# Kernel optimization log

Hardware: AMD Instinct MI355X
Metric: run time of the kernel (lower is better)

## Reference

```python
import jax, jax.numpy as jnp
import numpy as np

D_PROJ = 256
SCALE = D_PROJ ** (-0.5)


def setup_inputs() -> dict:
    key = jax.random.key(0)
    k1, k2, k3, k4 = jax.random.split(key, 4)
    B, L, Dh = 16, 2048, 1280
    T, Dg = 512, 768
    H = jax.random.normal(k1, (B, L, Dh), dtype=jnp.float32)
    G = jax.random.normal(k2, (B, T, Dg), dtype=jnp.float32)
    # Linear weights (torch nn.Linear: out = x @ W.T), small init to keep softmax well-conditioned
    Wq = jax.random.normal(k3, (D_PROJ, Dg), dtype=jnp.float32) * 0.02
    Wk = jax.random.normal(k4, (D_PROJ, Dh), dtype=jnp.float32) * 0.02
    return {"H": H, "G": G, "Wq": Wq, "Wk": Wk}


def reference(H, G, Wq, Wk):
    # Q = Wq(G): [B,T,P]; K = Wk(H): [B,L,P]
    Q = jnp.einsum('btg,pg->btp', G, Wq)
    K = jnp.einsum('bld,pd->blp', H, Wk)
    # The torch module's chunked online-softmax computes exact softmax over L.
    logits = jnp.einsum('btp,blp->btl', Q, K) * SCALE  # [B,T,L]
    A = jax.nn.softmax(logits, axis=-1)
    # Values are the raw residue embeddings H (not projected).
    Z = jnp.einsum('btl,bld->btd', A, H)  # [B,T,Dh]
    return Z
```

## Files before the change

### kernel.cpp

```cpp
#include <hip/hip_runtime.h>
#include <stdint.h>

typedef __attribute__((ext_vector_type(8))) short   short8;
typedef __attribute__((ext_vector_type(8))) __bf16  bf16x8;
typedef __attribute__((ext_vector_type(4))) float   floatx4;

#define DEV static __device__ __forceinline__

DEV unsigned short f2b(float f) {
  union { float f; unsigned u; } v; v.f = f;
  unsigned u = v.u;
  unsigned r = u + 0x7FFFu + ((u >> 16) & 1u);
  return (unsigned short)(r >> 16);
}
DEV float b2f(unsigned short s) {
  union { unsigned u; float f; } v; v.u = ((unsigned)s) << 16;
  return v.f;
}

DEV void gload_lds16(const void* g, void* l) {
  __builtin_amdgcn_global_load_lds(
      (const __attribute__((address_space(1))) unsigned int*)g,
      (__attribute__((address_space(3))) unsigned int*)l,
      16, 0, 0);
}

__global__ void cvt_kernel(const float* __restrict__ in, unsigned short* __restrict__ out, int n4) {
  int i = blockIdx.x * blockDim.x + threadIdx.x;
  if (i >= n4) return;
  float4 v = ((const float4*)in)[i];
  ushort4 o;
  o.x = f2b(v.x); o.y = f2b(v.y); o.z = f2b(v.z); o.w = f2b(v.w);
  ((ushort4*)out)[i] = o;
}

__global__ void transpose_cvt_H(const float* __restrict__ H, unsigned short* __restrict__ HT) {
  __shared__ unsigned short tile[64 * 68];
  const int b  = blockIdx.z;
  const int l0 = blockIdx.x * 64;
  const int d0 = blockIdx.y * 64;
  const int t  = threadIdx.x;

  {
    int row = t >> 2;
    int seg = t & 3;
    const float* src = H + ((size_t)b * 2048 + l0 + row) * 1280 + d0 + seg * 16;
#pragma unroll
    for (int s = 0; s < 4; ++s) {
      float4 v = *(const float4*)(src + s * 4);
      ushort4 o;
      o.x = f2b(v.x); o.y = f2b(v.y); o.z = f2b(v.z); o.w = f2b(v.w);
      *(ushort4*)&tile[row * 68 + seg * 16 + s * 4] = o;
    }
  }
  __syncthreads();
  {
    int dr = t >> 2;
    int ls = (t & 3) * 16;
    unsigned short* dst = HT + ((size_t)b * 1280 + d0 + dr) * 2048 + l0 + ls;
    short8 a, c;
#pragma unroll
    for (int i = 0; i < 8; ++i) a[i] = (short)tile[(ls + i) * 68 + dr];
#pragma unroll
    for (int i = 0; i < 8; ++i) c[i] = (short)tile[(ls + 8 + i) * 68 + dr];
    *(short8*)dst = a;
    *(short8*)(dst + 8) = c;
  }
}

__global__ void rowsum_inv_kernel(const unsigned short* __restrict__ E, float* __restrict__ linv, int rowlen) {
  int row  = blockIdx.x * 4 + (threadIdx.x >> 6);
  int lane = threadIdx.x & 63;
  const unsigned short* p = E + (size_t)row * rowlen;
  float s = 0.f;
  for (int c = lane * 8; c < rowlen; c += 512) {
    short8 v = *(const short8*)(p + c);
#pragma unroll
    for (int k = 0; k < 8; ++k) s += b2f((unsigned short)v[k]);
  }
#pragma unroll
  for (int off = 32; off > 0; off >>= 1) s += __shfl_down(s, off, 64);
  if (lane == 0) linv[row] = 1.0f / s;
}

template <int AMODE>
__global__ void proj_gemm(const void* __restrict__ Apv, const unsigned short* __restrict__ Bt,
                          unsigned short* __restrict__ C, int K, int lda) {
  __shared__ unsigned short As[64 * 32];
  __shared__ unsigned short Bs[256 * 32];

  const int m0   = blockIdx.x * 64;
  const int t    = threadIdx.x;
  const int lane = t & 63;
  const int wave = t >> 6;
  const int wn   = wave * 64;
  const int r16  = lane & 15;
  const int q    = lane >> 4;

  const unsigned short* Abf = (const unsigned short*)Apv;
  const float* A32 = (const float*)Apv;

  floatx4 acc[4][4];
#pragma unroll
  for (int i = 0; i < 4; ++i)
#pragma unroll
    for (int j = 0; j < 4; ++j) acc[i][j] = (floatx4){0.f, 0.f, 0.f, 0.f};

  for (int kt = 0; kt < K; kt += 32) {
    __syncthreads();
#pragma unroll
    for (int cc = 0; cc < 4; ++cc) {
      int c = t + cc * 256;
      gload_lds16(Bt + (size_t)(c >> 2) * K + kt + (c & 3) * 8, &Bs[c * 8]);
    }
    if constexpr (AMODE == 0) {
      gload_lds16(Abf + (size_t)(m0 + (t >> 2)) * lda + kt + (t & 3) * 8, &As[t * 8]);
    } else {
      const float* g = A32 + (size_t)(m0 + (t >> 2)) * lda + kt + (t & 3) * 8;
      float4 v0 = *(const float4*)g;
      float4 v1 = *(const float4*)(g + 4);
      short8 p;
      p[0] = (short)f2b(v0.x); p[1] = (short)f2b(v0.y);
      p[2] = (short)f2b(v0.z); p[3] = (short)f2b(v0.w);
      p[4] = (short)f2b(v1.x); p[5] = (short)f2b(v1.y);
      p[6] = (short)f2b(v1.z); p[7] = (short)f2b(v1.w);
      *(short8*)&As[t * 8] = p;
    }
    __syncthreads();

    bf16x8 af[4], bfr[4];
#pragma unroll
    for (int i = 0; i < 4; ++i) af[i]  = *(const bf16x8*)&As[(i * 16 + r16) * 32 + q * 8];
#pragma unroll
    for (int j = 0; j < 4; ++j) bfr[j] = *(const bf16x8*)&Bs[(wn + j * 16 + r16) * 32 + q * 8];
#pragma unroll
    for (int i = 0; i < 4; ++i)
#pragma unroll
      for (int j = 0; j < 4; ++j)
        acc[i][j] = __builtin_amdgcn_mfma_f32_16x16x32_bf16(af[i], bfr[j], acc[i][j], 0, 0, 0);
  }

#pragma unroll
  for (int i = 0; i < 4; ++i) {
#pragma unroll
    for (int r = 0; r < 4; ++r) {
      int m = m0 + i * 16 + q * 4 + r;
#pragma unroll
      for (int j = 0; j < 4; ++j) {
        int n = wn + j * 16 + r16;
        C[(size_t)m * 256 + n] = f2b(acc[i][j][r]);
      }
    }
  }
}

template <int EPI>
__global__ void gemm_nt(const unsigned short* __restrict__ Ab, const unsigned short* __restrict__ Btb,
                        void* __restrict__ Cpv, const float* __restrict__ linvb,
                        int K, int lda, int ldb, int ldc,
                        long long sA, long long sB, long long sC, int sL, float escale) {
  __shared__ unsigned short As[128 * 32];
  __shared__ unsigned short Bs[128 * 32];

  const int bz  = blockIdx.z;
  const int m0  = blockIdx.y * 128;
  const int n0  = blockIdx.x * 128;
  const int t   = threadIdx.x;
  const int lane = t & 63;
  const int wave = t >> 6;
  const int wm  = (wave & 1) * 64;
  const int wn  = (wave >> 1) * 64;
  const int r16 = lane & 15;
  const int q   = lane >> 4;

  const unsigned short* Bt = Btb + (long long)bz * sB;
  const unsigned short* A  = Ab + (long long)bz * sA;

  floatx4 acc[4][4];
#pragma unroll
  for (int i = 0; i < 4; ++i)
#pragma unroll
    for (int j = 0; j < 4; ++j) acc[i][j] = (floatx4){0.f, 0.f, 0.f, 0.f};

  for (int kt = 0; kt < K; kt += 32) {
    __syncthreads();
#pragma unroll
    for (int cc = 0; cc < 2; ++cc) {
      int c = t + cc * 256;
      gload_lds16(Bt + (size_t)(n0 + (c >> 2)) * ldb + kt + (c & 3) * 8, &Bs[c * 8]);
    }
#pragma unroll
    for (int cc = 0; cc < 2; ++cc) {
      int c = t + cc * 256;
      gload_lds16(A + (size_t)(m0 + (c >> 2)) * lda + kt + (c & 3) * 8, &As[c * 8]);
    }
    __syncthreads();

    bf16x8 af[4], bfr[4];
#pragma unroll
    for (int i = 0; i < 4; ++i) af[i]  = *(const bf16x8*)&As[(wm + i * 16 + r16) * 32 + q * 8];
#pragma unroll
    for (int j = 0; j < 4; ++j) bfr[j] = *(const bf16x8*)&Bs[(wn + j * 16 + r16) * 32 + q * 8];
#pragma unroll
    for (int i = 0; i < 4; ++i)
#pragma unroll
      for (int j = 0; j < 4; ++j)
        acc[i][j] = __builtin_amdgcn_mfma_f32_16x16x32_bf16(af[i], bfr[j], acc[i][j], 0, 0, 0);
  }

  if constexpr (EPI == 1) {
    unsigned short* C = (unsigned short*)Cpv + (long long)bz * sC;
#pragma unroll
    for (int i = 0; i < 4; ++i) {
#pragma unroll
      for (int r = 0; r < 4; ++r) {
        int m = m0 + wm + i * 16 + q * 4 + r;
#pragma unroll
        for (int j = 0; j < 4; ++j) {
          int n = n0 + wn + j * 16 + r16;
          C[(size_t)m * ldc + n] = f2b(__expf(acc[i][j][r] * escale));
        }
      }
    }
  } else {
    float* C = (float*)Cpv + (long long)bz * sC;
    const float* linv = linvb + (long long)bz * sL;
#pragma unroll
    for (int i = 0; i < 4; ++i) {
#pragma unroll
      for (int r = 0; r < 4; ++r) {
        int m = m0 + wm + i * 16 + q * 4 + r;
        float sc = linv[m];
#pragma unroll
        for (int j = 0; j < 4; ++j) {
          int n = n0 + wn + j * 16 + r16;
          C[(size_t)m * ldc + n] = acc[i][j][r] * sc;
        }
      }
    }
  }
}

extern "C" void kernel_launch(void* const* d_in, const int* in_sizes, int n_in,
                              void* d_out, int out_size, void* d_ws, size_t ws_size,
                              hipStream_t stream) {
  (void)in_sizes; (void)n_in; (void)out_size; (void)ws_size;
  const float* H  = (const float*)d_in[0];
  const float* G  = (const float*)d_in[1];
  const float* Wq = (const float*)d_in[2];
  const float* Wk = (const float*)d_in[3];
  float* Z = (float*)d_out;

  constexpr int B = 16, L = 2048, Dh = 1280, T = 512, Dg = 768, P = 256;

  char* ws = (char*)d_ws;
  size_t off = 0;
  auto alloc = [&](size_t bytes) { void* p = ws + off; off += (bytes + 255) & ~(size_t)255; return p; };
  unsigned short* Gbf  = (unsigned short*)alloc((size_t)B * T * Dg * 2);
  unsigned short* Wqbf = (unsigned short*)alloc((size_t)P * Dg * 2);
  unsigned short* Wkbf = (unsigned short*)alloc((size_t)P * Dh * 2);
  unsigned short* Qbf  = (unsigned short*)alloc((size_t)B * T * P * 2);
  unsigned short* Kbf  = (unsigned short*)alloc((size_t)B * L * P * 2);
  unsigned short* HT   = (unsigned short*)alloc((size_t)B * Dh * L * 2);
  unsigned short* E    = (unsigned short*)alloc((size_t)B * T * L * 2);
  float*          linv = (float*)alloc((size_t)B * T * 4);

  cvt_kernel<<<(B * T * Dg / 4 + 255) / 256, 256, 0, stream>>>(G, Gbf, B * T * Dg / 4);
  cvt_kernel<<<(P * Dg / 4 + 255) / 256, 256, 0, stream>>>(Wq, Wqbf, P * Dg / 4);
  cvt_kernel<<<(P * Dh / 4 + 255) / 256, 256, 0, stream>>>(Wk, Wkbf, P * Dh / 4);
  transpose_cvt_H<<<dim3(L / 64, Dh / 64, B), 256, 0, stream>>>(H, HT);

  proj_gemm<0><<<B * T / 64, 256, 0, stream>>>(Gbf, Wqbf, Qbf, Dg, Dg);
  proj_gemm<1><<<B * L / 64, 256, 0, stream>>>(H, Wkbf, Kbf, Dh, Dh);
  gemm_nt<1><<<dim3(L / 128, T / 128, B), 256, 0, stream>>>(
      Qbf, Kbf, E, nullptr, P, P, P, L,
      (long long)T * P, (long long)L * P, (long long)T * L, 0, 0.0625f);
  rowsum_inv_kernel<<<B * T / 4, 256, 0, stream>>>(E, linv, L);
  gemm_nt<2><<<dim3(Dh / 128, T / 128, B), 256, 0, stream>>>(
      E, HT, Z, linv, P * 0 + L, L, L, Dh,
      (long long)T * L, (long long)Dh * L, (long long)T * Dh, T, 0.f);
}
```

Baseline: 472.8 us.

## Fuse softmax row sums into exp GEMM epilogue and remap blocks per XCD

After: 444.2 us. 6.1% less time.

```diff
diff --git a/kernel.cpp b/kernel.cpp
--- a/kernel.cpp
+++ b/kernel.cpp
@@ -13,10 +13,6 @@
   unsigned r = u + 0x7FFFu + ((u >> 16) & 1u);
   return (unsigned short)(r >> 16);
 }
-DEV float b2f(unsigned short s) {
-  union { unsigned u; float f; } v; v.u = ((unsigned)s) << 16;
-  return v.f;
-}
 
 DEV void gload_lds16(const void* g, void* l) {
   __builtin_amdgcn_global_load_lds(
@@ -25,17 +21,28 @@
       16, 0, 0);
 }
 
-__global__ void cvt_kernel(const float* __restrict__ in, unsigned short* __restrict__ out, int n4) {
+__global__ void cvt3_kernel(const float* __restrict__ a, unsigned short* __restrict__ oa, int na4,
+                            const float* __restrict__ b, unsigned short* __restrict__ ob, int nb4,
+                            const float* __restrict__ c, unsigned short* __restrict__ oc, int nc4) {
   int i = blockIdx.x * blockDim.x + threadIdx.x;
-  if (i >= n4) return;
-  float4 v = ((const float4*)in)[i];
+  const float* src; unsigned short* dst; int k;
+  if (i < na4)                { src = a; dst = oa; k = i; }
+  else if (i < na4 + nb4)     { src = b; dst = ob; k = i - na4; }
+  else if (i < na4 + nb4 + nc4) { src = c; dst = oc; k = i - na4 - nb4; }
+  else return;
+  float4 v = ((const float4*)src)[k];
   ushort4 o;
   o.x = f2b(v.x); o.y = f2b(v.y); o.z = f2b(v.z); o.w = f2b(v.w);
-  ((ushort4*)out)[i] = o;
+  ((ushort4*)dst)[k] = o;
+}
+
+__global__ void zero_kernel(float* __restrict__ p, int n) {
+  int i = blockIdx.x * blockDim.x + threadIdx.x;
+  if (i < n) p[i] = 0.f;
 }
 
 __global__ void transpose_cvt_H(const float* __restrict__ H, unsigned short* __restrict__ HT) {
-  __shared__ unsigned short tile[64 * 68];
+  __shared__ unsigned short tile[64 * 66];
   const int b  = blockIdx.z;
   const int l0 = blockIdx.x * 64;
   const int d0 = blockIdx.y * 64;
@@ -45,12 +52,14 @@
     int row = t >> 2;
     int seg = t & 3;
     const float* src = H + ((size_t)b * 2048 + l0 + row) * 1280 + d0 + seg * 16;
+    unsigned short* trow = &tile[row * 66 + seg * 16];
 #pragma unroll
     for (int s = 0; s < 4; ++s) {
       float4 v = *(const float4*)(src + s * 4);
-      ushort4 o;
-      o.x = f2b(v.x); o.y = f2b(v.y); o.z = f2b(v.z); o.w = f2b(v.w);
-      *(ushort4*)&tile[row * 68 + seg * 16 + s * 4] = o;
+      ushort2 p0 = { f2b(v.x), f2b(v.y) };
+      ushort2 p1 = { f2b(v.z), f2b(v.w) };
+      *(ushort2*)&trow[s * 4]     = p0;
+      *(ushort2*)&trow[s * 4 + 2] = p1;
     }
   }
   __syncthreads();
@@ -60,27 +69,12 @@
     unsigned short* dst = HT + ((size_t)b * 1280 + d0 + dr) * 2048 + l0 + ls;
     short8 a, c;
 #pragma unroll
-    for (int i = 0; i < 8; ++i) a[i] = (short)tile[(ls + i) * 68 + dr];
-#pragma unroll
-    for (int i = 0; i < 8; ++i) c[i] = (short)tile[(ls + 8 + i) * 68 + dr];
+    for (int i = 0; i < 8; ++i) a[i] = (short)tile[(ls + i) * 66 + dr];
+#pragma unroll
+    for (int i = 0; i < 8; ++i) c[i] = (short)tile[(ls + 8 + i) * 66 + dr];
     *(short8*)dst = a;
     *(short8*)(dst + 8) = c;
   }
-}
-
-__global__ void rowsum_inv_kernel(const unsigned short* __restrict__ E, float* __restrict__ linv, int rowlen) {
-  int row  = blockIdx.x * 4 + (threadIdx.x >> 6);
-  int lane = threadIdx.x & 63;
-  const unsigned short* p = E + (size_t)row * rowlen;
-  float s = 0.f;
-  for (int c = lane * 8; c < rowlen; c += 512) {
-    short8 v = *(const short8*)(p + c);
-#pragma unroll
-    for (int k = 0; k < 8; ++k) s += b2f((unsigned short)v[k]);
-  }
-#pragma unroll
-  for (int off = 32; off > 0; off >>= 1) s += __shfl_down(s, off, 64);
-  if (lane == 0) linv[row] = 1.0f / s;
 }
 
 template <int AMODE>
@@ -156,22 +150,28 @@
 
 template <int EPI>
 __global__ void gemm_nt(const unsigned short* __restrict__ Ab, const unsigned short* __restrict__ Btb,
-                        void* __restrict__ Cpv, const float* __restrict__ linvb,
+                        void* __restrict__ Cpv, float* __restrict__ sums,
                         int K, int lda, int ldb, int ldc,
-                        long long sA, long long sB, long long sC, int sL, float escale) {
+                        long long sA, long long sB, long long sC, int sstride,
+                        float escale, int nx, int tiles_pb) {
   __shared__ unsigned short As[128 * 32];
   __shared__ unsigned short Bs[128 * 32];
 
-  const int bz  = blockIdx.z;
-  const int m0  = blockIdx.y * 128;
-  const int n0  = blockIdx.x * 128;
-  const int t   = threadIdx.x;
+  const int g   = blockIdx.x;
+  const int xcd = g & 7;
+  const int jj  = g >> 3;
+  const int bz  = xcd * 2 + jj / tiles_pb;
+  const int tt  = jj % tiles_pb;
+  const int m0  = (tt / nx) * 128;
+  const int n0  = (tt % nx) * 128;
+
+  const int t    = threadIdx.x;
   const int lane = t & 63;
   const int wave = t >> 6;
-  const int wm  = (wave & 1) * 64;
-  const int wn  = (wave >> 1) * 64;
-  const int r16 = lane & 15;
-  const int q   = lane >> 4;
+  const int wm   = (wave & 1) * 64;
+  const int wn   = (wave >> 1) * 64;
+  const int r16  = lane & 15;
+  const int q    = lane >> 4;
 
   const unsigned short* Bt = Btb + (long long)bz * sB;
   const unsigned short* A  = Ab + (long long)bz * sA;
@@ -215,22 +215,28 @@
 #pragma unroll
       for (int r = 0; r < 4; ++r) {
         int m = m0 + wm + i * 16 + q * 4 + r;
+        float ps = 0.f;
 #pragma unroll
         for (int j = 0; j < 4; ++j) {
           int n = n0 + wn + j * 16 + r16;
-          C[(size_t)m * ldc + n] = f2b(__expf(acc[i][j][r] * escale));
+          float v = __expf(acc[i][j][r] * escale);
+          ps += v;
+          C[(size_t)m * ldc + n] = f2b(v);
         }
+#pragma unroll
+        for (int msk = 1; msk < 16; msk <<= 1) ps += __shfl_xor(ps, msk, 64);
+        if (r16 == 0) atomicAdd(&sums[(long long)bz * sstride + m], ps);
       }
     }
   } else {
     float* C = (float*)Cpv + (long long)bz * sC;
-    const float* linv = linvb + (long long)bz * sL;
+    const float* sb = sums + (long long)bz * sstride;
 #pragma unroll
     for (int i = 0; i < 4; ++i) {
 #pragma unroll
       for (int r = 0; r < 4; ++r) {
         int m = m0 + wm + i * 16 + q * 4 + r;
-        float sc = linv[m];
+        float sc = 1.0f / sb[m];
 #pragma unroll
         for (int j = 0; j < 4; ++j) {
           int n = n0 + wn + j * 16 + r16;
@@ -263,20 +269,26 @@
   unsigned short* Kbf  = (unsigned short*)alloc((size_t)B * L * P * 2);
   unsigned short* HT   = (unsigned short*)alloc((size_t)B * Dh * L * 2);
   unsigned short* E    = (unsigned short*)alloc((size_t)B * T * L * 2);
-  float*          linv = (float*)alloc((size_t)B * T * 4);
-
-  cvt_kernel<<<(B * T * Dg / 4 + 255) / 256, 256, 0, stream>>>(G, Gbf, B * T * Dg / 4);
-  cvt_kernel<<<(P * Dg / 4 + 255) / 256, 256, 0, stream>>>(Wq, Wqbf, P * Dg / 4);
-  cvt_kernel<<<(P * Dh / 4 + 255) / 256, 256, 0, stream>>>(Wk, Wkbf, P * Dh / 4);
+  float*          sums = (float*)alloc((size_t)B * T * 4);
+
+  {
+    int na4 = B * T * Dg / 4, nb4 = P * Dg / 4, nc4 = P * Dh / 4;
+    cvt3_kernel<<<(na4 + nb4 + nc4 + 255) / 256, 256, 0, stream>>>(
+        G, Gbf, na4, Wq, Wqbf, nb4, Wk, Wkbf, nc4);
+  }
+  zero_kernel<<<(B * T + 255) / 256, 256, 0, stream>>>(sums, B * T);
   transpose_cvt_H<<<dim3(L / 64, Dh / 64, B), 256, 0, stream>>>(H, HT);
 
   proj_gemm<0><<<B * T / 64, 256, 0, stream>>>(Gbf, Wqbf, Qbf, Dg, Dg);
   proj_gemm<1><<<B * L / 64, 256, 0, stream>>>(H, Wkbf, Kbf, Dh, Dh);
-  gemm_nt<1><<<dim3(L / 128, T / 128, B), 256, 0, stream>>>(
-      Qbf, Kbf, E, nullptr, P, P, P, L,
-      (long long)T * P, (long long)L * P, (long long)T * L, 0, 0.0625f);
-  rowsum_inv_kernel<<<B * T / 4, 256, 0, stream>>>(E, linv, L);
-  gemm_nt<2><<<dim3(Dh / 128, T / 128, B), 256, 0, stream>>>(
-      E, HT, Z, linv, P * 0 + L, L, L, Dh,
-      (long long)T * L, (long long)Dh * L, (long long)T * Dh, T, 0.f);
-}
+
+  gemm_nt<1><<<B * (T / 128) * (L / 128), 256, 0, stream>>>(
+      Qbf, Kbf, E, sums, P, P, P, L,
+      (long long)T * P, (long long)L * P, (long long)T * L, T,
+      0.0625f, L / 128, (T / 128) * (L / 128));
+
+  gemm_nt<2><<<B * (T / 128) * (Dh / 128), 256, 0, stream>>>(
+      E, HT, Z, sums, L, L, L, Dh,
+      (long long)T * L, (long long)Dh * L, (long long)T * Dh, T,
+      0.f, Dh / 128, (T / 128) * (Dh / 128));
+}
```
